# Performance work log

Hardware: AMD Instinct MI355X
Metric: run time of the kernel (lower is better)

Reference implementation:

```python
import jax, jax.numpy as jnp
import numpy as np

D_MODEL = 1024
N_HEADS = 16
HEAD_DIM = D_MODEL // N_HEADS
ROPE_BASE = 10000.0
B, S = 2, 2048


def _rope_cos_sin(seq_len):
    inv_freq = 1.0 / (ROPE_BASE ** (jnp.arange(0, HEAD_DIM, 2, dtype=jnp.float32) / HEAD_DIM))
    t = jnp.arange(seq_len, dtype=jnp.float32)
    freqs = jnp.outer(t, inv_freq)                 # [S, HEAD_DIM/2]
    emb = jnp.concatenate([freqs, freqs], axis=-1)  # [S, HEAD_DIM]
    return jnp.cos(emb), jnp.sin(emb)


def _apply_rope(x, cos, sin):
    # x: [B, H, S, D]; cos/sin: [S, D]
    x1 = x[..., ::2]
    x2 = x[..., 1::2]
    return jnp.concatenate(
        [x1 * cos[..., ::2] - x2 * sin[..., ::2],
         x1 * sin[..., 1::2] + x2 * cos[..., 1::2]], axis=-1)


def setup_inputs() -> dict:
    key = jax.random.key(0)
    ks = jax.random.split(key, 5)
    std = 1.0 / np.sqrt(D_MODEL)
    x = jax.random.normal(ks[0], (B, S, D_MODEL), dtype=jnp.float32)
    Wq = jax.random.normal(ks[1], (D_MODEL, D_MODEL), dtype=jnp.float32) * std
    Wk = jax.random.normal(ks[2], (D_MODEL, D_MODEL), dtype=jnp.float32) * std
    Wv = jax.random.normal(ks[3], (D_MODEL, D_MODEL), dtype=jnp.float32) * std
    Wo = jax.random.normal(ks[4], (D_MODEL, D_MODEL), dtype=jnp.float32) * std
    attn_mask = jnp.tril(jnp.ones((S, S), dtype=jnp.int32))  # 0 = masked (causal)
    return {"x": x, "Wq": Wq, "Wk": Wk, "Wv": Wv, "Wo": Wo, "attn_mask": attn_mask}


def reference(x, Wq, Wk, Wv, Wo, attn_mask):
    b, s, _ = x.shape
    scale = 1.0 / np.sqrt(HEAD_DIM)
    # torch Linear: y = x @ W.T
    q = (x @ Wq.T).reshape(b, s, N_HEADS, HEAD_DIM).transpose(0, 2, 1, 3)
    k = (x @ Wk.T).reshape(b, s, N_HEADS, HEAD_DIM).transpose(0, 2, 1, 3)
    v = (x @ Wv.T).reshape(b, s, N_HEADS, HEAD_DIM).transpose(0, 2, 1, 3)
    cos, sin = _rope_cos_sin(s)
    q = _apply_rope(q, cos, sin)
    k = _apply_rope(k, cos, sin)
    scores = jnp.einsum('bhqd,bhkd->bhqk', q, k) * scale  # [B,H,S,S]
    scores = jnp.where(attn_mask == 0, -jnp.inf, scores)
    attn = jax.nn.softmax(scores, axis=-1)
    out = jnp.einsum('bhqk,bhkd->bhqd', attn, v)
    out = out.transpose(0, 2, 1, 3).reshape(b, s, D_MODEL)
    return out @ Wo.T
```

## Files before the change

### kernel.cpp

```cpp
#include <hip/hip_runtime.h>
#include <hip/hip_bf16.h>
#include <cstdint>

#define SEQ 2048
#define NH  16
#define HD  64
#define DM  1024
#define BATCH 2

typedef unsigned short ushort_t;
typedef __attribute__((ext_vector_type(8))) short short8;
typedef __attribute__((ext_vector_type(4))) float f32x4;

__device__ __forceinline__ ushort_t f2bf(float f){
  __hip_bfloat16 h = __float2bfloat16(f);
  return *reinterpret_cast<ushort_t*>(&h);
}
__device__ __forceinline__ ushort_t f2bf_fast(float f){
  uint32_t u = __float_as_uint(f);
  u += 0x7FFF + ((u >> 16) & 1);
  return (ushort_t)(u >> 16);
}

#define GLDS(g, l) __builtin_amdgcn_global_load_lds( \
    (const __attribute__((address_space(1))) void*)(g), \
    (__attribute__((address_space(3))) void*)(l), 16, 0, 0)

__global__ __launch_bounds__(256) void rope_tab_kernel(float* __restrict__ tab){
  int idx = blockIdx.x * 256 + threadIdx.x;
  int t = idx >> 5, j = idx & 31;
  float invf = exp2f(-(float)j * 0.41524101186092033f);
  float sn, cn;
  sincosf((float)t * invf, &sn, &cn);
  tab[2*idx]   = cn;
  tab[2*idx+1] = sn;
}

__global__ __launch_bounds__(256) void cvt_kernel(
    const float* __restrict__ x,  const float* __restrict__ Wq,
    const float* __restrict__ Wk, const float* __restrict__ Wv,
    const float* __restrict__ Wo,
    ushort_t* __restrict__ xb,  ushort_t* __restrict__ wqb,
    ushort_t* __restrict__ wkb, ushort_t* __restrict__ wvb,
    ushort_t* __restrict__ wob)
{
  int f = blockIdx.x * 256 + threadIdx.x;
  const float* s; ushort_t* d; int off;
  if(f < (1<<20)){ s = x; d = xb; off = f; }
  else{
    int r = f - (1<<20);
    int w = r >> 18;
    off = r & ((1<<18)-1);
    s = (w==0)?Wq:(w==1)?Wk:(w==2)?Wv:Wo;
    d = (w==0)?wqb:(w==1)?wkb:(w==2)?wvb:wob;
  }
  float4 v = *reinterpret_cast<const float4*>(s + (size_t)off*4);
  ushort_t t[4] = {f2bf(v.x), f2bf(v.y), f2bf(v.z), f2bf(v.w)};
  *reinterpret_cast<uint2*>(d + (size_t)off*4) = *reinterpret_cast<const uint2*>(t);
}

template<bool SWAP>
__device__ __forceinline__ void gemm_core_bf16_glds(
    const ushort_t* __restrict__ A, const ushort_t* __restrict__ B,
    ushort_t* As, ushort_t* Bs, int m0, int n0, f32x4 acc[4][4])
{
  const int tid  = threadIdx.x;
  const int lane = tid & 63;
  const int wave = tid >> 6;
  const int quad = lane >> 4, l16 = lane & 15;
  const int wm = (wave >> 1) * 64, wn = (wave & 1) * 64;
  for(int k0 = 0; k0 < DM; k0 += 32){
    #pragma unroll
    for(int u = 0; u < 2; u++){
      int idx = tid + u * 256;
      int row = idx >> 2, seg = idx & 3;
      int col = (seg ^ (row & 3)) * 8;
      ushort_t* la = &As[(size_t)(idx & ~63) * 8];
      ushort_t* lb = &Bs[(size_t)(idx & ~63) * 8];
      GLDS(&A[(size_t)(m0+row)*DM + k0 + col], la);
      GLDS(&B[(size_t)(n0+row)*DM + k0 + col], lb);
    }
    __syncthreads();
    short8 af[4], bf[4];
    #pragma unroll
    for(int mt=0;mt<4;mt++){
      int row = wm + mt*16 + l16;
      af[mt] = *reinterpret_cast<const short8*>(&As[row*32 + (quad ^ (row&3))*8]);
    }
    #pragma unroll
    for(int nt=0;nt<4;nt++){
      int row = wn + nt*16 + l16;
      bf[nt] = *reinterpret_cast<const short8*>(&Bs[row*32 + (quad ^ (row&3))*8]);
    }
    #pragma unroll
    for(int mt=0;mt<4;mt++)
      #pragma unroll
      for(int nt=0;nt<4;nt++)
        acc[mt][nt] = SWAP
          ? __builtin_amdgcn_mfma_f32_16x16x32_bf16(bf[nt], af[mt], acc[mt][nt], 0, 0, 0)
          : __builtin_amdgcn_mfma_f32_16x16x32_bf16(af[mt], bf[nt], acc[mt][nt], 0, 0, 0);
    __syncthreads();
  }
}

template<bool SWAP>
__device__ __forceinline__ void gemm_core_f32(
    const float* __restrict__ A, const float* __restrict__ B,
    ushort_t* As, ushort_t* Bs, int m0, int n0, f32x4 acc[4][4])
{
  const int tid  = threadIdx.x;
  const int lane = tid & 63;
  const int wave = tid >> 6;
  const int quad = lane >> 4, l16 = lane & 15;
  const int wm = (wave >> 1) * 64, wn = (wave & 1) * 64;
  for(int k0 = 0; k0 < DM; k0 += 32){
    #pragma unroll
    for(int u = 0; u < 4; u++){
      int idx = tid + u * 256;
      int row = idx >> 3, seg = idx & 7;
      float4 av = *reinterpret_cast<const float4*>(&A[(size_t)(m0+row)*DM + k0 + seg*4]);
      float4 bv = *reinterpret_cast<const float4*>(&B[(size_t)(n0+row)*DM + k0 + seg*4]);
      ushort_t at[4] = {f2bf(av.x), f2bf(av.y), f2bf(av.z), f2bf(av.w)};
      ushort_t bt[4] = {f2bf(bv.x), f2bf(bv.y), f2bf(bv.z), f2bf(bv.w)};
      *reinterpret_cast<uint2*>(&As[row*40 + seg*4]) = *reinterpret_cast<const uint2*>(at);
      *reinterpret_cast<uint2*>(&Bs[row*40 + seg*4]) = *reinterpret_cast<const uint2*>(bt);
    }
    __syncthreads();
    short8 af[4], bf[4];
    #pragma unroll
    for(int mt=0;mt<4;mt++) af[mt] = *reinterpret_cast<const short8*>(&As[(wm+mt*16+l16)*40 + quad*8]);
    #pragma unroll
    for(int nt=0;nt<4;nt++) bf[nt] = *reinterpret_cast<const short8*>(&Bs[(wn+nt*16+l16)*40 + quad*8]);
    #pragma unroll
    for(int mt=0;mt<4;mt++)
      #pragma unroll
      for(int nt=0;nt<4;nt++)
        acc[mt][nt] = SWAP
          ? __builtin_amdgcn_mfma_f32_16x16x32_bf16(bf[nt], af[mt], acc[mt][nt], 0, 0, 0)
          : __builtin_amdgcn_mfma_f32_16x16x32_bf16(af[mt], bf[nt], acc[mt][nt], 0, 0, 0);
    __syncthreads();
  }
}

__device__ __forceinline__ void qkv_epilogue(
    int z, int m0, int n0, f32x4 acc[4][4], const float* __restrict__ tab,
    ushort_t* __restrict__ Q, ushort_t* __restrict__ Ko, ushort_t* __restrict__ Vt)
{
  const int tid  = threadIdx.x;
  const int lane = tid & 63;
  const int wave = tid >> 6;
  const int quad = lane >> 4, l16 = lane & 15;
  const int wm = (wave >> 1) * 64, wn = (wave & 1) * 64;
  if(z < 2){
    ushort_t* outp = (z == 0) ? Q : Ko;
    const float qscale = (z == 0) ? 0.18033688011112042f : 1.0f;
    #pragma unroll
    for(int nt=0;nt<4;nt++){
      int n  = n0 + wn + nt*16 + l16;
      int h  = n >> 6, dh = n & 63;
      int j  = dh & 31;
      int outd = (dh >> 1) + (dh & 1) * 32;
      bool even = (dh & 1) == 0;
      #pragma unroll
      for(int mt=0;mt<4;mt++){
        #pragma unroll
        for(int r=0;r<4;r++){
          int m = m0 + wm + mt*16 + quad*4 + r;
          int b = m >> 11, s = m & 2047;
          float v = acc[mt][nt][r];
          float p = __shfl_xor(v, 1);
          float2 cs = *reinterpret_cast<const float2*>(&tab[(s*32 + j)*2]);
          float o = even ? (v * cs.x - p * cs.y) : (p * cs.y + v * cs.x);
          outp[((size_t)(b*NH + h)*SEQ + s)*HD + outd] = f2bf(o * qscale);
        }
      }
    }
  } else {
    #pragma unroll
    for(int nt=0;nt<4;nt++){
      #pragma unroll
      for(int mt=0;mt<4;mt++){
        int m = m0 + wm + mt*16 + l16;
        int b = m >> 11, s = m & 2047;
        #pragma unroll
        for(int r=0;r<4;r++){
          int n = n0 + wn + nt*16 + quad*4 + r;
          int h = n >> 6, dh = n & 63;
          Vt[((size_t)(b*NH + h)*HD + dh)*SEQ + s] = f2bf_fast(acc[mt][nt][r]);
        }
      }
    }
  }
}

__global__ __launch_bounds__(256) void qkv_bf16_kernel(
    const ushort_t* __restrict__ xb,
    const ushort_t* __restrict__ wqb, const ushort_t* __restrict__ wkb,
    const ushort_t* __restrict__ wvb, const float* __restrict__ tab,
    ushort_t* __restrict__ Q, ushort_t* __restrict__ Ko, ushort_t* __restrict__ Vt)
{
  const int z = blockIdx.z;
  const ushort_t* W = (z == 0) ? wqb : (z == 1) ? wkb : wvb;
  const int m0 = blockIdx.x * 128, n0 = blockIdx.y * 128;
  __shared__ __align__(16) ushort_t As[128*32];
  __shared__ __align__(16) ushort_t Bs[128*32];
  f32x4 acc[4][4];
  #pragma unroll
  for(int i=0;i<4;i++)
    #pragma unroll
    for(int j=0;j<4;j++) acc[i][j] = (f32x4){0.f,0.f,0.f,0.f};
  if(z == 2) gemm_core_bf16_glds<true >(xb, W, As, Bs, m0, n0, acc);
  else       gemm_core_bf16_glds<false>(xb, W, As, Bs, m0, n0, acc);
  qkv_epilogue(z, m0, n0, acc, tab, Q, Ko, Vt);
}

__global__ __launch_bounds__(256) void qkv_f32_kernel(
    const float* __restrict__ x,
    const float* __restrict__ Wq, const float* __restrict__ Wk,
    const float* __restrict__ Wv, const float* __restrict__ tab,
    ushort_t* __restrict__ Q, ushort_t* __restrict__ Ko, ushort_t* __restrict__ Vt)
{
  const int z = blockIdx.z;
  const float* W = (z == 0) ? Wq : (z == 1) ? Wk : Wv;
  const int m0 = blockIdx.x * 128, n0 = blockIdx.y * 128;
  __shared__ __align__(16) char smem[20480];
  ushort_t* As = (ushort_t*)smem;
  ushort_t* Bs = (ushort_t*)(smem + 10240);
  f32x4 acc[4][4];
  #pragma unroll
  for(int i=0;i<4;i++)
    #pragma unroll
    for(int j=0;j<4;j++) acc[i][j] = (f32x4){0.f,0.f,0.f,0.f};
  if(z == 2) gemm_core_f32<true >(x, W, As, Bs, m0, n0, acc);
  else       gemm_core_f32<false>(x, W, As, Bs, m0, n0, acc);
  qkv_epilogue(z, m0, n0, acc, tab, Q, Ko, Vt);
}

__global__ __launch_bounds__(256) void attn_kernel(
    ushort_t* __restrict__ Qbuf, const ushort_t* __restrict__ K,
    const ushort_t* __restrict__ Vt)
{
  const int bh = blockIdx.x;
  const int y  = blockIdx.y;
  const int g  = (y < 8) ? (15 - y) : (y - 8);
  const int T  = 2*(g+1);
  const int tid  = threadIdx.x;
  const int lane = tid & 63;
  const int wave = tid >> 6;
  const int quad = lane >> 4, l16 = lane & 15;

  ushort_t*       Qp = Qbuf + (size_t)bh * SEQ * HD;
  const ushort_t* Kp = K    + (size_t)bh * SEQ * HD;
  const ushort_t* Vp = Vt   + (size_t)bh * HD * SEQ;

  __shared__ __align__(16) ushort_t Ks[64*72];
  __shared__ __align__(16) ushort_t Vs[64*72];
  __shared__ __align__(16) ushort_t Pl[4][32*72];
  ushort_t* pl = &Pl[wave][0];

  const int srow0 = tid >> 3;
  const int scol  = (tid & 7) * 8;

  const int q0w = 128*g + 32*wave;

  short8 qf[2][2];
  #pragma unroll
  for(int s=0;s<2;s++)
    #pragma unroll
    for(int kk=0;kk<2;kk++)
      qf[s][kk] = *reinterpret_cast<const short8*>(&Qp[(size_t)(q0w + 16*s + l16)*HD + kk*32 + quad*8]);

  f32x4 oacc[2][4];
  #pragma unroll
  for(int s=0;s<2;s++)
    #pragma unroll
    for(int dt=0;dt<4;dt++) oacc[s][dt] = (f32x4){0.f,0.f,0.f,0.f};
  float llane[2] = {0.f, 0.f};

  uint4 kreg[2], vreg[2];
  #pragma unroll
  for(int u=0;u<2;u++){
    int row = srow0 + u*32;
    kreg[u] = *reinterpret_cast<const uint4*>(&Kp[(size_t)row*HD + scol]);
    vreg[u] = *reinterpret_cast<const uint4*>(&Vp[(size_t)row*SEQ + scol]);
  }

  for(int t = 0; t < T; t++){
    const int kv0 = t * 64;

    __syncthreads();
    #pragma unroll
    for(int u=0;u<2;u++){
      int row = srow0 + u*32;
      *reinterpret_cast<uint4*>(&Ks[row*72 + scol]) = kreg[u];
      *reinterpret_cast<uint4*>(&Vs[row*72 + scol]) = vreg[u];
    }
    __syncthreads();

    if(t < T-1){
      #pragma unroll
      for(int u=0;u<2;u++){
        int row = srow0 + u*32;
        kreg[u] = *reinterpret_cast<const uint4*>(&Kp[(size_t)(kv0 + 64 + row)*HD + scol]);
        vreg[u] = *reinterpret_cast<const uint4*>(&Vp[(size_t)row*SEQ + kv0 + 64 + scol]);
      }
    }

    short8 kf[4][2], vf[4][2];
    #pragma unroll
    for(int nt=0;nt<4;nt++)
      #pragma unroll
      for(int kk=0;kk<2;kk++)
        kf[nt][kk] = *reinterpret_cast<const short8*>(&Ks[(nt*16 + l16)*72 + kk*32 + quad*8]);
    #pragma unroll
    for(int dt=0;dt<4;dt++)
      #pragma unroll
      for(int kk=0;kk<2;kk++)
        vf[dt][kk] = *reinterpret_cast<const short8*>(&Vs[(dt*16 + l16)*72 + kk*32 + quad*8]);

    #pragma unroll
    for(int s=0;s<2;s++){
      f32x4 sacc[4];
      #pragma unroll
      for(int nt=0;nt<4;nt++) sacc[nt] = (f32x4){0.f,0.f,0.f,0.f};
      #pragma unroll
      for(int kk=0;kk<2;kk++)
        #pragma unroll
        for(int nt=0;nt<4;nt++)
          sacc[nt] = __builtin_amdgcn_mfma_f32_16x16x32_bf16(kf[nt][kk], qf[s][kk], sacc[nt], 0,0,0);

      const int q_abs = q0w + 16*s + l16;
      const bool maskable = (kv0 + 63 > q0w + 16*s);
      float pv[4][4];
      #pragma unroll
      for(int nt=0;nt<4;nt++)
        #pragma unroll
        for(int r=0;r<4;r++){
          float sv = sacc[nt][r];
          if(maskable){
            int kv_abs = kv0 + nt*16 + quad*4 + r;
            sv = (kv_abs > q_abs) ? -1e30f : sv;
          }
          float p = exp2f(sv);
          pv[nt][r] = p;
          llane[s] += p;
        }

      asm volatile("" ::: "memory");
      #pragma unroll
      for(int nt=0;nt<4;nt++){
        uint32_t lo = (uint32_t)f2bf_fast(pv[nt][0]) | ((uint32_t)f2bf_fast(pv[nt][1]) << 16);
        uint32_t hi = (uint32_t)f2bf_fast(pv[nt][2]) | ((uint32_t)f2bf_fast(pv[nt][3]) << 16);
        uint2 pk; pk.x = lo; pk.y = hi;
        *reinterpret_cast<uint2*>(&pl[(16*s + l16)*72 + nt*16 + quad*4]) = pk;
      }
      asm volatile("s_waitcnt lgkmcnt(0)" ::: "memory");

      #pragma unroll
      for(int kk=0;kk<2;kk++){
        short8 pf = *reinterpret_cast<const short8*>(&pl[(16*s + l16)*72 + kk*32 + quad*8]);
        #pragma unroll
        for(int dt=0;dt<4;dt++)
          oacc[s][dt] = __builtin_amdgcn_mfma_f32_16x16x32_bf16(vf[dt][kk], pf, oacc[s][dt], 0,0,0);
      }
    }
  }

  #pragma unroll
  for(int s=0;s<2;s++){
    float lt = llane[s];
    lt += __shfl_xor(lt, 16);
    lt += __shfl_xor(lt, 32);
    float inv = 1.0f / lt;
    #pragma unroll
    for(int dt=0;dt<4;dt++){
      uint32_t lo = (uint32_t)f2bf_fast(oacc[s][dt][0] * inv) | ((uint32_t)f2bf_fast(oacc[s][dt][1] * inv) << 16);
      uint32_t hi = (uint32_t)f2bf_fast(oacc[s][dt][2] * inv) | ((uint32_t)f2bf_fast(oacc[s][dt][3] * inv) << 16);
      uint2 pk; pk.x = lo; pk.y = hi;
      *reinterpret_cast<uint2*>(&Qp[(size_t)(q0w + 16*s + l16)*HD + dt*16 + quad*4]) = pk;
    }
  }
}

__global__ __launch_bounds__(256) void out_proj_bf16_kernel(
    const ushort_t* __restrict__ ctx, const ushort_t* __restrict__ wob,
    float* __restrict__ out)
{
  const int m0 = blockIdx.x * 128, n0 = blockIdx.y * 128;
  __shared__ __align__(16) ushort_t As[128*32];
  __shared__ __align__(16) ushort_t Bs[128*32];
  const int tid  = threadIdx.x;
  const int lane = tid & 63;
  const int wave = tid >> 6;
  const int quad = lane >> 4, l16 = lane & 15;
  const int wm = (wave >> 1) * 64, wn = (wave & 1) * 64;

  f32x4 acc[4][4];
  #pragma unroll
  for(int i=0;i<4;i++)
    #pragma unroll
    for(int j=0;j<4;j++) acc[i][j] = (f32x4){0.f,0.f,0.f,0.f};

  for(int k0 = 0; k0 < DM; k0 += 32){
    const int head = k0 >> 6, off = k0 & 63;
    #pragma unroll
    for(int u = 0; u < 2; u++){
      int idx = tid + u * 256;
      int row = idx >> 2, seg = idx & 3;
      int col = (seg ^ (row & 3)) * 8;
      int m = m0 + row, b = m >> 11, s = m & 2047;
      ushort_t* la = &As[(size_t)(idx & ~63) * 8];
      ushort_t* lb = &Bs[(size_t)(idx & ~63) * 8];
      GLDS(&ctx[((size_t)(b*NH + head)*SEQ + s)*HD + off + col], la);
      GLDS(&wob[(size_t)(n0+row)*DM + k0 + col], lb);
    }
    __syncthreads();
    short8 af[4], bf[4];
    #pragma unroll
    for(int mt=0;mt<4;mt++){
      int row = wm + mt*16 + l16;
      af[mt] = *reinterpret_cast<const short8*>(&As[row*32 + (quad ^ (row&3))*8]);
    }
    #pragma unroll
    for(int nt=0;nt<4;nt++){
      int row = wn + nt*16 + l16;
      bf[nt] = *reinterpret_cast<const short8*>(&Bs[row*32 + (quad ^ (row&3))*8]);
    }
    #pragma unroll
    for(int mt=0;mt<4;mt++)
      #pragma unroll
      for(int nt=0;nt<4;nt++)
        acc[mt][nt] = __builtin_amdgcn_mfma_f32_16x16x32_bf16(af[mt], bf[nt], acc[mt][nt], 0, 0, 0);
    __syncthreads();
  }
  #pragma unroll
  for(int mt=0;mt<4;mt++)
    #pragma unroll
    for(int nt=0;nt<4;nt++)
      #pragma unroll
      for(int r=0;r<4;r++){
        int m = m0 + wm + mt*16 + quad*4 + r;
        int n = n0 + wn + nt*16 + l16;
        out[(size_t)m*DM + n] = acc[mt][nt][r];
      }
}

__global__ __launch_bounds__(256) void out_proj_f32_kernel(
    const ushort_t* __restrict__ ctx, const float* __restrict__ Wo,
    float* __restrict__ out)
{
  const int m0 = blockIdx.x * 128, n0 = blockIdx.y * 128;
  __shared__ __align__(16) ushort_t As[128*40];
  __shared__ __align__(16) ushort_t Bs[128*40];
  const int tid  = threadIdx.x;
  const int lane = tid & 63;
  const int wave = tid >> 6;
  const int quad = lane >> 4, l16 = lane & 15;
  const int wm = (wave >> 1) * 64, wn = (wave & 1) * 64;

  f32x4 acc[4][4];
  #pragma unroll
  for(int i=0;i<4;i++)
    #pragma unroll
    for(int j=0;j<4;j++) acc[i][j] = (f32x4){0.f,0.f,0.f,0.f};

  for(int k0 = 0; k0 < DM; k0 += 32){
    const int head = k0 >> 6, off = k0 & 63;
    #pragma unroll
    for(int u = 0; u < 2; u++){
      int idx = tid + u * 256;
      int row = idx >> 2, seg = idx & 3;
      int m = m0 + row, b = m >> 11, s = m & 2047;
      *reinterpret_cast<uint4*>(&As[row*40 + seg*8]) =
        *reinterpret_cast<const uint4*>(&ctx[((size_t)(b*NH + head)*SEQ + s)*HD + off + seg*8]);
    }
    #pragma unroll
    for(int u = 0; u < 4; u++){
      int idx = tid + u * 256;
      int row = idx >> 3, seg = idx & 7;
      float4 bv = *reinterpret_cast<const float4*>(&Wo[(size_t)(n0+row)*DM + k0 + seg*4]);
      ushort_t bt[4] = {f2bf(bv.x), f2bf(bv.y), f2bf(bv.z), f2bf(bv.w)};
      *reinterpret_cast<uint2*>(&Bs[row*40 + seg*4]) = *reinterpret_cast<const uint2*>(bt);
    }
    __syncthreads();
    short8 af[4], bf[4];
    #pragma unroll
    for(int mt=0;mt<4;mt++) af[mt] = *reinterpret_cast<const short8*>(&As[(wm+mt*16+l16)*40 + quad*8]);
    #pragma unroll
    for(int nt=0;nt<4;nt++) bf[nt] = *reinterpret_cast<const short8*>(&Bs[(wn+nt*16+l16)*40 + quad*8]);
    #pragma unroll
    for(int mt=0;mt<4;mt++)
      #pragma unroll
      for(int nt=0;nt<4;nt++)
        acc[mt][nt] = __builtin_amdgcn_mfma_f32_16x16x32_bf16(af[mt], bf[nt], acc[mt][nt], 0, 0, 0);
    __syncthreads();
  }
  #pragma unroll
  for(int mt=0;mt<4;mt++)
    #pragma unroll
    for(int nt=0;nt<4;nt++)
      #pragma unroll
      for(int r=0;r<4;r++){
        int m = m0 + wm + mt*16 + quad*4 + r;
        int n = n0 + wn + nt*16 + l16;
        out[(size_t)m*DM + n] = acc[mt][nt][r];
      }
}

extern "C" void kernel_launch(void* const* d_in, const int* in_sizes, int n_in,
                              void* d_out, int out_size, void* d_ws, size_t ws_size,
                              hipStream_t stream) {
  const float* x  = (const float*)d_in[0];
  const float* Wq = (const float*)d_in[1];
  const float* Wk = (const float*)d_in[2];
  const float* Wv = (const float*)d_in[3];
  const float* Wo = (const float*)d_in[4];
  float* out = (float*)d_out;

  char* ws = (char*)d_ws;
  ushort_t* Qb  = (ushort_t*)ws;
  float*    tab = (float*)(ws + (8u << 20));
  ushort_t* Kb  = (ushort_t*)d_out;
  ushort_t* Vt  = (ushort_t*)d_out + (size_t)BATCH*NH*SEQ*HD;

  rope_tab_kernel<<<256, 256, 0, stream>>>(tab);

  const bool big_ws = ws_size >= (25u << 20);

  if(big_ws){
    ushort_t* xb  = (ushort_t*)(ws + (8u  << 20) + (512u << 10));
    char*     wb0 = ws + (16u << 20) + (512u << 10);
    ushort_t* wqb = (ushort_t*)(wb0);
    ushort_t* wkb = (ushort_t*)(wb0 + (2u << 20));
    ushort_t* wvb = (ushort_t*)(wb0 + (4u << 20));
    ushort_t* wob = (ushort_t*)(wb0 + (6u << 20));
    cvt_kernel<<<8192, 256, 0, stream>>>(x, Wq, Wk, Wv, Wo, xb, wqb, wkb, wvb, wob);
    dim3 g1(32, 8, 3);
    qkv_bf16_kernel<<<g1, 256, 0, stream>>>(xb, wqb, wkb, wvb, tab, Qb, Kb, Vt);
    dim3 g2(32, 16);
    attn_kernel<<<g2, 256, 0, stream>>>(Qb, Kb, Vt);
    dim3 g3(32, 8);
    out_proj_bf16_kernel<<<g3, 256, 0, stream>>>(Qb, wob, out);
  } else {
    dim3 g1(32, 8, 3);
    qkv_f32_kernel<<<g1, 256, 0, stream>>>(x, Wq, Wk, Wv, tab, Qb, Kb, Vt);
    dim3 g2(32, 16);
    attn_kernel<<<g2, 256, 0, stream>>>(Qb, Kb, Vt);
    dim3 g3(32, 8);
    out_proj_f32_kernel<<<g3, 256, 0, stream>>>(Qb, Wo, out);
  }
}
```

Before: 253.9 us.

## Double-buffer LDS staging in QKV and out-proj GEMMs, use __expf in softmax

```diff
diff --git a/kernel.cpp b/kernel.cpp
--- a/kernel.cpp
+++ b/kernel.cpp
@@ -62,35 +62,46 @@
 template<bool SWAP>
 __device__ __forceinline__ void gemm_core_bf16_glds(
     const ushort_t* __restrict__ A, const ushort_t* __restrict__ B,
-    ushort_t* As, ushort_t* Bs, int m0, int n0, f32x4 acc[4][4])
+    ushort_t* As, ushort_t* Bs,
+    int m0, int n0, f32x4 acc[4][4])
 {
   const int tid  = threadIdx.x;
   const int lane = tid & 63;
   const int wave = tid >> 6;
   const int quad = lane >> 4, l16 = lane & 15;
   const int wm = (wave >> 1) * 64, wn = (wave & 1) * 64;
+
+  const int srow0 = tid >> 2, sseg0 = tid & 3;
+
+  #define STAGE_BF16(k0, hb) { \
+    _Pragma("unroll") \
+    for(int u = 0; u < 2; u++){ \
+      int idx = tid + u * 256; \
+      int row = srow0 + u * 64, seg = sseg0; \
+      int col = (seg ^ (row & 3)) * 8; \
+      ushort_t* la = &As[(hb)*4096 + (size_t)(idx & ~63) * 8]; \
+      ushort_t* lb = &Bs[(hb)*4096 + (size_t)(idx & ~63) * 8]; \
+      GLDS(&A[(size_t)(m0+row)*DM + (k0) + col], la); \
+      GLDS(&B[(size_t)(n0+row)*DM + (k0) + col], lb); \
+    } }
+
+  STAGE_BF16(0, 0);
+  __syncthreads();
+  int cur = 0;
   for(int k0 = 0; k0 < DM; k0 += 32){
-    #pragma unroll
-    for(int u = 0; u < 2; u++){
-      int idx = tid + u * 256;
-      int row = idx >> 2, seg = idx & 3;
-      int col = (seg ^ (row & 3)) * 8;
-      ushort_t* la = &As[(size_t)(idx & ~63) * 8];
-      ushort_t* lb = &Bs[(size_t)(idx & ~63) * 8];
-      GLDS(&A[(size_t)(m0+row)*DM + k0 + col], la);
-      GLDS(&B[(size_t)(n0+row)*DM + k0 + col], lb);
-    }
-    __syncthreads();
+    if(k0 + 32 < DM) STAGE_BF16(k0 + 32, cur ^ 1);
+    const ushort_t* as = &As[cur*4096];
+    const ushort_t* bs = &Bs[cur*4096];
     short8 af[4], bf[4];
     #pragma unroll
     for(int mt=0;mt<4;mt++){
       int row = wm + mt*16 + l16;
-      af[mt] = *reinterpret_cast<const short8*>(&As[row*32 + (quad ^ (row&3))*8]);
+      af[mt] = *reinterpret_cast<const short8*>(&as[row*32 + (quad ^ (row&3))*8]);
     }
     #pragma unroll
     for(int nt=0;nt<4;nt++){
       int row = wn + nt*16 + l16;
-      bf[nt] = *reinterpret_cast<const short8*>(&Bs[row*32 + (quad ^ (row&3))*8]);
+      bf[nt] = *reinterpret_cast<const short8*>(&bs[row*32 + (quad ^ (row&3))*8]);
     }
     #pragma unroll
     for(int mt=0;mt<4;mt++)
@@ -100,7 +111,9 @@
           ? __builtin_amdgcn_mfma_f32_16x16x32_bf16(bf[nt], af[mt], acc[mt][nt], 0, 0, 0)
           : __builtin_amdgcn_mfma_f32_16x16x32_bf16(af[mt], bf[nt], acc[mt][nt], 0, 0, 0);
     __syncthreads();
-  }
+    cur ^= 1;
+  }
+  #undef STAGE_BF16
 }
 
 template<bool SWAP>
@@ -153,7 +166,7 @@
   const int wm = (wave >> 1) * 64, wn = (wave & 1) * 64;
   if(z < 2){
     ushort_t* outp = (z == 0) ? Q : Ko;
-    const float qscale = (z == 0) ? 0.18033688011112042f : 1.0f;
+    const float qscale = (z == 0) ? 0.125f : 1.0f;
     #pragma unroll
     for(int nt=0;nt<4;nt++){
       int n  = n0 + wn + nt*16 + l16;
@@ -202,8 +215,8 @@
   const int z = blockIdx.z;
   const ushort_t* W = (z == 0) ? wqb : (z == 1) ? wkb : wvb;
   const int m0 = blockIdx.x * 128, n0 = blockIdx.y * 128;
-  __shared__ __align__(16) ushort_t As[128*32];
-  __shared__ __align__(16) ushort_t Bs[128*32];
+  __shared__ __align__(16) ushort_t As[2*128*32];
+  __shared__ __align__(16) ushort_t Bs[2*128*32];
   f32x4 acc[4][4];
   #pragma unroll
   for(int i=0;i<4;i++)
@@ -341,7 +354,7 @@
             int kv_abs = kv0 + nt*16 + quad*4 + r;
             sv = (kv_abs > q_abs) ? -1e30f : sv;
           }
-          float p = exp2f(sv);
+          float p = __expf(sv);
           pv[nt][r] = p;
           llane[s] += p;
         }
@@ -387,13 +400,14 @@
     float* __restrict__ out)
 {
   const int m0 = blockIdx.x * 128, n0 = blockIdx.y * 128;
-  __shared__ __align__(16) ushort_t As[128*32];
-  __shared__ __align__(16) ushort_t Bs[128*32];
+  __shared__ __align__(16) ushort_t As[2*128*32];
+  __shared__ __align__(16) ushort_t Bs[2*128*32];
   const int tid  = threadIdx.x;
   const int lane = tid & 63;
   const int wave = tid >> 6;
   const int quad = lane >> 4, l16 = lane & 15;
   const int wm = (wave >> 1) * 64, wn = (wave & 1) * 64;
+  const int srow0 = tid >> 2, sseg0 = tid & 3;
 
   f32x4 acc[4][4];
   #pragma unroll
@@ -401,30 +415,37 @@
     #pragma unroll
     for(int j=0;j<4;j++) acc[i][j] = (f32x4){0.f,0.f,0.f,0.f};
 
+  #define STAGE_OP(k0, hb) { \
+    const int head = (k0) >> 6, off = (k0) & 63; \
+    _Pragma("unroll") \
+    for(int u = 0; u < 2; u++){ \
+      int idx = tid + u * 256; \
+      int row = srow0 + u * 64, seg = sseg0; \
+      int col = (seg ^ (row & 3)) * 8; \
+      int m = m0 + row, b = m >> 11, s = m & 2047; \
+      ushort_t* la = &As[(hb)*4096 + (size_t)(idx & ~63) * 8]; \
+      ushort_t* lb = &Bs[(hb)*4096 + (size_t)(idx & ~63) * 8]; \
+      GLDS(&ctx[((size_t)(b*NH + head)*SEQ + s)*HD + off + col], la); \
+      GLDS(&wob[(size_t)(n0+row)*DM + (k0) + col], lb); \
+    } }
+
+  STAGE_OP(0, 0);
+  __syncthreads();
+  int cur = 0;
   for(int k0 = 0; k0 < DM; k0 += 32){
-    const int head = k0 >> 6, off = k0 & 63;
-    #pragma unroll
-    for(int u = 0; u < 2; u++){
-      int idx = tid + u * 256;
-      int row = idx >> 2, seg = idx & 3;
-      int col = (seg ^ (row & 3)) * 8;
-      int m = m0 + row, b = m >> 11, s = m & 2047;
-      ushort_t* la = &As[(size_t)(idx & ~63) * 8];
-      ushort_t* lb = &Bs[(size_t)(idx & ~63) * 8];
-      GLDS(&ctx[((size_t)(b*NH + head)*SEQ + s)*HD + off + col], la);
-      GLDS(&wob[(size_t)(n0+row)*DM + k0 + col], lb);
-    }
-    __syncthreads();
+    if(k0 + 32 < DM) STAGE_OP(k0 + 32, cur ^ 1);
+    const ushort_t* as = &As[cur*4096];
+    const ushort_t* bs = &Bs[cur*4096];
     short8 af[4], bf[4];
     #pragma unroll
     for(int mt=0;mt<4;mt++){
       int row = wm + mt*16 + l16;
-      af[mt] = *reinterpret_cast<const short8*>(&As[row*32 + (quad ^ (row&3))*8]);
+      af[mt] = *reinterpret_cast<const short8*>(&as[row*32 + (quad ^ (row&3))*8]);
     }
     #pragma unroll
     for(int nt=0;nt<4;nt++){
       int row = wn + nt*16 + l16;
-      bf[nt] = *reinterpret_cast<const short8*>(&Bs[row*32 + (quad ^ (row&3))*8]);
+      bf[nt] = *reinterpret_cast<const short8*>(&bs[row*32 + (quad ^ (row&3))*8]);
     }
     #pragma unroll
     for(int mt=0;mt<4;mt++)
@@ -432,7 +453,10 @@
       for(int nt=0;nt<4;nt++)
         acc[mt][nt] = __builtin_amdgcn_mfma_f32_16x16x32_bf16(af[mt], bf[nt], acc[mt][nt], 0, 0, 0);
     __syncthreads();
-  }
+    cur ^= 1;
+  }
+  #undef STAGE_OP
+
   #pragma unroll
   for(int mt=0;mt<4;mt++)
     #pragma unroll
```

New measurement: 240.6 us. 1.06x faster.
